# Kernel tuning notes

Measured on AMD Instinct MI355X. Metric: run time of the kernel, lower is better.

Reference implementation:

```python
import jax, jax.numpy as jnp
import numpy as np

NUM_USERS = 50000
NUM_ITEMS = 10000
FACTORS = 200
COMPONENTS = 36
FEAT_DIM = 512
HC = 64  # layers_component[0]
HI = 64  # layers_item[0]
B = 256
L = 32   # positives per user (fixed-length stand-in for ragged)


def setup_inputs() -> dict:
    key = jax.random.key(0)
    ks = jax.random.split(key, 20)
    g = lambda k, shape, s=0.01: (jax.random.normal(k, shape, dtype=jnp.float32) * s)
    glorot = lambda k, shape: jax.random.normal(k, shape, dtype=jnp.float32) * np.sqrt(2.0 / (shape[0] + shape[-1]))
    return {
        "user": jax.random.randint(ks[0], (B,), 0, NUM_USERS),
        "item": jax.random.randint(ks[1], (B,), 0, NUM_ITEMS),
        "user_pos": jax.random.randint(ks[2], (B, L), 0, NUM_ITEMS),
        "Gu": g(ks[3], (NUM_USERS, FACTORS)),
        "Gi": g(ks[4], (NUM_ITEMS, FACTORS)),
        "Pi": g(ks[5], (NUM_ITEMS, FACTORS)),
        "Fi": g(ks[6], (NUM_ITEMS, COMPONENTS, FEAT_DIM), 0.1),
        # component attention weights
        "cW0u": glorot(ks[7], (FACTORS, HC)),
        "cW0i": glorot(ks[8], (FEAT_DIM, HC)),
        "cb0": glorot(ks[9], (1, HC))[0],
        "cW1": glorot(ks[10], (HC, 1)),
        "cb1": glorot(ks[11], (1, 1))[0],
        # item attention weights
        "iW0u": glorot(ks[12], (FACTORS, HI)),
        "iW0iv": glorot(ks[13], (FACTORS, HI)),
        "iW0ip": glorot(ks[14], (FACTORS, HI)),
        "iW0ix": glorot(ks[15], (FEAT_DIM, HI)),
        "ib0": glorot(ks[16], (1, HI))[0],
        "iW1": glorot(ks[17], (HI, 1)),
        "ib1": glorot(ks[18], (1, 1))[0],
    }


def reference(user, item, user_pos, Gu, Gi, Pi, Fi,
              cW0u, cW0i, cb0, cW1, cb1,
              iW0u, iW0iv, iW0ip, iW0ix, ib0, iW1, ib1):
    gu = Gu[user]            # [B, F]
    gi = Gi[item]            # [B, F]
    pi = Pi[item]            # [B, F]
    g_pos = Gi[user_pos]     # [B, L, F]
    p_pos = Pi[user_pos]     # [B, L, F]
    f_pos = Fi[user_pos]     # [B, L, C, D]

    # --- component-level attention ---
    b = jax.nn.relu(jnp.einsum('bf,fh->bh', gu, cW0u)[:, None, None, :]
                    + jnp.einsum('blcd,dh->blch', f_pos, cW0i)
                    + cb0)                               # [B, L, C, HC]
    b = jnp.einsum('blch,ho->blco', b, cW1) + cb1        # [B, L, C, 1]
    b = jax.nn.softmax(b, axis=2)                        # softmax over components
    x = jnp.sum(b * f_pos, axis=2)                       # [B, L, D]

    # --- item-level attention ---
    a = jax.nn.relu(jnp.einsum('bf,fh->bh', gu, iW0u)[:, None, :]
                    + jnp.einsum('blf,fh->blh', g_pos, iW0iv)
                    + jnp.einsum('blf,fh->blh', p_pos, iW0ip)
                    + jnp.einsum('bld,dh->blh', x, iW0ix)
                    + ib0)                               # [B, L, HI]
    a = jnp.einsum('blh,ho->blo', a, iW1) + ib1          # [B, L, 1]
    # Faithful to original: softmax over flat-values axis 1 (size-1 last dim -> ones)
    a = jax.nn.softmax(a, axis=-1)
    all_a = jnp.sum(a * p_pos, axis=1)                   # [B, F]

    gu_p = gu + all_a
    xui = jnp.sum(gu_p * gi, axis=1)                     # [B]
    return (xui, gu, gi, pi)
```

## Files before the change

kernel.cpp:

```cpp
#include <hip/hip_runtime.h>


#define BB   256
#define LL   32
#define FF   200

__global__ __launch_bounds__(256) void acf_kernel(
    const int*   __restrict__ user,
    const int*   __restrict__ item,
    const int*   __restrict__ user_pos,
    const float* __restrict__ Gu,
    const float* __restrict__ Gi,
    const float* __restrict__ Pi,
    float* __restrict__ out)
{
    const int b = blockIdx.x;
    const int t = threadIdx.x;

    __shared__ int   s_pos[LL];
    __shared__ float s_red[4];

    if (t < LL) s_pos[t] = user_pos[b * LL + t];
    __syncthreads();

    const int u  = user[b];
    const int it = item[b];

    float partial = 0.0f;
    if (t < FF) {
        const float gu = Gu[(size_t)u  * FF + t];
        const float gi = Gi[(size_t)it * FF + t];
        const float pi = Pi[(size_t)it * FF + t];

        float* out_gu = out + BB;
        float* out_gi = out + BB + BB * FF;
        float* out_pi = out + BB + 2 * BB * FF;
        out_gu[b * FF + t] = gu;
        out_gi[b * FF + t] = gi;
        out_pi[b * FF + t] = pi;

        float alla = 0.0f;
        #pragma unroll
        for (int l = 0; l < LL; ++l) {
            alla += Pi[(size_t)s_pos[l] * FF + t];
        }
        partial = (gu + alla) * gi;
    }

    #pragma unroll
    for (int off = 32; off > 0; off >>= 1)
        partial += __shfl_down(partial, off, 64);

    const int wave = t >> 6;
    const int lane = t & 63;
    if (lane == 0) s_red[wave] = partial;
    __syncthreads();
    if (t == 0) {
        out[b] = s_red[0] + s_red[1] + s_red[2] + s_red[3];
    }
}

extern "C" void kernel_launch(void* const* d_in, const int* in_sizes, int n_in,
                              void* d_out, int out_size, void* d_ws, size_t ws_size,
                              hipStream_t stream) {
    const int*   user     = (const int*)  d_in[0];
    const int*   item     = (const int*)  d_in[1];
    const int*   user_pos = (const int*)  d_in[2];
    const float* Gu       = (const float*)d_in[3];
    const float* Gi       = (const float*)d_in[4];
    const float* Pi       = (const float*)d_in[5];
    float* out = (float*)d_out;

    acf_kernel<<<BB, 256, 0, stream>>>(user, item, user_pos, Gu, Gi, Pi, out);
}
```

Baseline: 9.948 us.

## Use single-wave blocks with float4 loads and shuffle-broadcast indices

Each block becomes one 64-lane wave in which every lane handles four features through float4 loads and stores. Gather indices are broadcast with wave shuffles instead of shared memory, and the cross-wave shared-memory reduction and barriers are removed. This cuts load instruction count and synchronisation in a latency-bound gather. In exchange, 14 of 64 lanes sit idle and there is less thread-level parallelism per block.

New measurement: 13.55 us, median of 2. 1.36x slower.

```diff
diff --git a/kernel.cpp b/kernel.cpp
--- a/kernel.cpp
+++ b/kernel.cpp
@@ -4,8 +4,9 @@
 #define BB   256
 #define LL   32
 #define FF   200
+#define NC   50
 
-__global__ __launch_bounds__(256) void acf_kernel(
+__global__ __launch_bounds__(64) void acf_kernel(
     const int*   __restrict__ user,
     const int*   __restrict__ item,
     const int*   __restrict__ user_pos,
@@ -14,50 +15,63 @@
     const float* __restrict__ Pi,
     float* __restrict__ out)
 {
-    const int b = blockIdx.x;
-    const int t = threadIdx.x;
-
-    __shared__ int   s_pos[LL];
-    __shared__ float s_red[4];
-
-    if (t < LL) s_pos[t] = user_pos[b * LL + t];
-    __syncthreads();
+    const int b    = blockIdx.x;
+    const int lane = threadIdx.x;
 
     const int u  = user[b];
     const int it = item[b];
 
-    float partial = 0.0f;
-    if (t < FF) {
-        const float gu = Gu[(size_t)u  * FF + t];
-        const float gi = Gi[(size_t)it * FF + t];
-        const float pi = Pi[(size_t)it * FF + t];
+    int myidx = (lane < LL) ? user_pos[b * LL + lane] : 0;
 
-        float* out_gu = out + BB;
-        float* out_gi = out + BB + BB * FF;
-        float* out_pi = out + BB + 2 * BB * FF;
-        out_gu[b * FF + t] = gu;
-        out_gi[b * FF + t] = gi;
-        out_pi[b * FF + t] = pi;
+    const float4* Gu4 = (const float4*)Gu;
+    const float4* Gi4 = (const float4*)Gi;
+    const float4* Pi4 = (const float4*)Pi;
 
-        float alla = 0.0f;
-        #pragma unroll
-        for (int l = 0; l < LL; ++l) {
-            alla += Pi[(size_t)s_pos[l] * FF + t];
+    const bool active = lane < NC;
+
+    float4 gu4 = make_float4(0.f, 0.f, 0.f, 0.f);
+    float4 gi4 = gu4, pi4 = gu4;
+    if (active) {
+        gu4 = Gu4[(size_t)u  * NC + lane];
+        gi4 = Gi4[(size_t)it * NC + lane];
+        pi4 = Pi4[(size_t)it * NC + lane];
+    }
+
+    int idx[LL];
+    #pragma unroll
+    for (int l = 0; l < LL; ++l) idx[l] = __shfl(myidx, l, 64);
+
+    float4 alla = make_float4(0.f, 0.f, 0.f, 0.f);
+    #pragma unroll
+    for (int l = 0; l < LL; ++l) {
+        if (active) {
+            float4 v = Pi4[(size_t)idx[l] * NC + lane];
+            alla.x += v.x; alla.y += v.y; alla.z += v.z; alla.w += v.w;
         }
-        partial = (gu + alla) * gi;
+    }
+
+    if (active) {
+        float4* out_gu = (float4*)(out + BB);
+        float4* out_gi = (float4*)(out + BB + BB * FF);
+        float4* out_pi = (float4*)(out + BB + 2 * BB * FF);
+        out_gu[b * NC + lane] = gu4;
+        out_gi[b * NC + lane] = gi4;
+        out_pi[b * NC + lane] = pi4;
+    }
+
+    float partial = 0.f;
+    if (active) {
+        partial = (gu4.x + alla.x) * gi4.x
+                + (gu4.y + alla.y) * gi4.y
+                + (gu4.z + alla.z) * gi4.z
+                + (gu4.w + alla.w) * gi4.w;
     }
 
     #pragma unroll
     for (int off = 32; off > 0; off >>= 1)
         partial += __shfl_down(partial, off, 64);
 
-    const int wave = t >> 6;
-    const int lane = t & 63;
-    if (lane == 0) s_red[wave] = partial;
-    __syncthreads();
-    if (t == 0) {
-        out[b] = s_red[0] + s_red[1] + s_red[2] + s_red[3];
-    }
+    if (lane == 0) out[b] = partial;
 }
 
 extern "C" void kernel_launch(void* const* d_in, const int* in_sizes, int n_in,
@@ -71,5 +85,5 @@
     const float* Pi       = (const float*)d_in[5];
     float* out = (float*)d_out;
 
-    acf_kernel<<<BB, 256, 0, stream>>>(user, item, user_pos, Gu, Gi, Pi, out);
+    acf_kernel<<<BB, 64, 0, stream>>>(user, item, user_pos, Gu, Gi, Pi, out);
 }
```
